# Optimization experiments

Hardware: AMD Instinct MI355X
Metric: run time of the kernel (lower is better)

The kernel has to match this reference:

```python
import jax, jax.numpy as jnp
import numpy as np

H, HKV, D = 32, 8, 128          # query heads, kv heads, head dim
G = H // HKV                     # GQA group size
PAGE, TOPK = 64, 64              # page size, top-k pages per (b, kv-head)
SCALE = D ** -0.5


def rotate_half(x):
    x1, x2 = x[..., : x.shape[-1] // 2], x[..., x.shape[-1] // 2 :]
    return jnp.concatenate((-x2, x1), axis=-1)


def setup_inputs() -> dict:
    key = jax.random.key(0)
    ks = jax.random.split(key, 8)
    B, Q, HID, S = 4, 1, 4096, 16384
    hidden_states = jax.random.normal(ks[0], (B, Q, HID), jnp.float32)
    # rotary embedding for current decode position S
    inv_freq = 1.0 / (10000.0 ** (np.arange(0, D, 2, dtype=np.float32) / D))
    ang = np.float32(S) * inv_freq
    emb = np.concatenate([ang, ang])  # [D]
    cos = jnp.broadcast_to(jnp.asarray(np.cos(emb))[None, None, :], (B, Q, D)).astype(jnp.float32)
    sin = jnp.broadcast_to(jnp.asarray(np.sin(emb))[None, None, :], (B, Q, D)).astype(jnp.float32)
    k_cache = jax.random.normal(ks[1], (B, HKV, S, D), jnp.float32)
    v_cache = jax.random.normal(ks[2], (B, HKV, S, D), jnp.float32)
    Wq = jax.random.normal(ks[3], (H * D, HID), jnp.float32) * 0.02
    Wk = jax.random.normal(ks[4], (HKV * D, HID), jnp.float32) * 0.02
    Wv = jax.random.normal(ks[5], (HKV * D, HID), jnp.float32) * 0.02
    Wo = jax.random.normal(ks[6], (HID, H * D), jnp.float32) * 0.02
    return dict(hidden_states=hidden_states, cos=cos, sin=sin,
                k_cache=k_cache, v_cache=v_cache, Wq=Wq, Wk=Wk, Wv=Wv, Wo=Wo)


def reference(hidden_states, cos, sin, k_cache, v_cache, Wq, Wk, Wv, Wo):
    B, Q, HID = hidden_states.shape
    S = k_cache.shape[2]
    P = S // PAGE

    # QKV projections (Linear, no bias) -> [B, heads, Q, D]
    q = (hidden_states @ Wq.T).reshape(B, Q, H, D).transpose(0, 2, 1, 3)
    k_new = (hidden_states @ Wk.T).reshape(B, Q, HKV, D).transpose(0, 2, 1, 3)
    v_new = (hidden_states @ Wv.T).reshape(B, Q, HKV, D).transpose(0, 2, 1, 3)

    # RoPE (unsqueeze_dim=1)
    c, s = cos[:, None, :, :], sin[:, None, :, :]
    q = q * c + rotate_half(q) * s
    k_new = k_new * c + rotate_half(k_new) * s

    # merge grouped query heads to kv heads (reduce='mean', merge_mode='kv')
    q_merged = q.reshape(B, HKV, G, Q, D).mean(axis=2)[:, :, 0, :]  # [B, HKV, D]

    # Quest page summaries: per-page elementwise min/max of keys
    Kp = k_cache.reshape(B, HKV, P, PAGE, D)
    Vp = v_cache.reshape(B, HKV, P, PAGE, D)
    kmin = Kp.min(axis=3)  # [B, HKV, P, D]
    kmax = Kp.max(axis=3)
    qm = q_merged[:, :, None, :]
    page_scores = jnp.maximum(qm * kmin, qm * kmax).sum(axis=-1)  # [B, HKV, P]

    # top-k page selection per (batch, kv head), gather selected pages
    _, idx = jax.lax.top_k(page_scores, TOPK)  # [B, HKV, TOPK]
    gidx = idx[:, :, :, None, None]
    K_sel = jnp.take_along_axis(Kp, gidx, axis=2).reshape(B, HKV, TOPK * PAGE, D)
    V_sel = jnp.take_along_axis(Vp, gidx, axis=2).reshape(B, HKV, TOPK * PAGE, D)

    # append current decode token's kv
    K = jnp.concatenate([K_sel, k_new], axis=2)  # [B, HKV, L, D]
    V = jnp.concatenate([V_sel, v_new], axis=2)

    # GQA attention over gathered sparse KV (no mask in quest decode path)
    qg = q.reshape(B, HKV, G, Q, D)
    logits = jnp.einsum('bhgqd,bhld->bhgql', qg, K) * SCALE
    w = jax.nn.softmax(logits.astype(jnp.float32), axis=-1).astype(q.dtype)
    o = jnp.einsum('bhgql,bhld->bhgqd', w, V)              # [B, HKV, G, Q, D]
    o = o.reshape(B, H, Q, D).transpose(0, 2, 1, 3).reshape(B, Q, H * D)
    return o @ Wo.T  # [B, Q, HID]
```

## Files before the change

### kernel.cpp

```cpp
#include <hip/hip_runtime.h>
#include <hip/hip_bf16.h>
#include <math.h>

constexpr int NB    = 4;
constexpr int NHID  = 4096;
constexpr int NHEAD = 32;
constexpr int NKV   = 8;
constexpr int NGQ   = 4;
constexpr int ND    = 128;
constexpr int NS    = 16384;
constexpr int NPG   = 64;
constexpr int NP    = 256;
constexpr int NTOP  = 64;
constexpr int NSPLIT = 32;
constexpr int PPS   = NTOP / NSPLIT;
constexpr float FSCALE = 0.08838834764831845f;

__global__ __launch_bounds__(256) void k_qkv(
    const float* __restrict__ hs, const float* __restrict__ Wq,
    const float* __restrict__ Wk, const float* __restrict__ Wv,
    float* __restrict__ qkv) {
  int row0 = blockIdx.x * 4;
  int t = threadIdx.x;
  const float4* x4 = (const float4*)hs;
  const float4* wr[4];
#pragma unroll
  for (int r = 0; r < 4; r++) {
    int row = row0 + r;
    const float* w;
    if (row < 4096)      w = Wq + (size_t)row * NHID;
    else if (row < 5120) w = Wk + (size_t)(row - 4096) * NHID;
    else                 w = Wv + (size_t)(row - 5120) * NHID;
    wr[r] = (const float4*)w;
  }
  float acc[4][4] = {};
  for (int j = t; j < NHID / 4; j += 256) {
    float4 x0 = x4[j], x1 = x4[1024 + j], x2 = x4[2048 + j], x3 = x4[3072 + j];
#pragma unroll
    for (int r = 0; r < 4; r++) {
      float4 w4 = wr[r][j];
      acc[r][0] += w4.x * x0.x + w4.y * x0.y + w4.z * x0.z + w4.w * x0.w;
      acc[r][1] += w4.x * x1.x + w4.y * x1.y + w4.z * x1.z + w4.w * x1.w;
      acc[r][2] += w4.x * x2.x + w4.y * x2.y + w4.z * x2.z + w4.w * x2.w;
      acc[r][3] += w4.x * x3.x + w4.y * x3.y + w4.z * x3.z + w4.w * x3.w;
    }
  }
  __shared__ float red[4][16];
  int lane = t & 63, wv = t >> 6;
#pragma unroll
  for (int r = 0; r < 4; r++)
#pragma unroll
    for (int b = 0; b < 4; b++) {
      float v = acc[r][b];
      v += __shfl_down(v, 32); v += __shfl_down(v, 16); v += __shfl_down(v, 8);
      v += __shfl_down(v, 4);  v += __shfl_down(v, 2);  v += __shfl_down(v, 1);
      if (lane == 0) red[wv][r * 4 + b] = v;
    }
  __syncthreads();
  if (t < 16) {
    int r = t >> 2, b = t & 3;
    float s = red[0][t] + red[1][t] + red[2][t] + red[3][t];
    qkv[(size_t)b * 6144 + row0 + r] = s;
  }
}

__global__ __launch_bounds__(256) void k_rope_merge(
    const float* __restrict__ qkv, const float* __restrict__ cosp,
    const float* __restrict__ sinp, float* __restrict__ qr,
    float* __restrict__ kn, float* __restrict__ vn, float* __restrict__ qm) {
  int b = blockIdx.x >> 3, kv = blockIdx.x & 7;
  const float* cs = cosp + b * ND;
  const float* sn = sinp + b * ND;
  int t = threadIdx.x;
  int g = t >> 6, i = t & 63;
  __shared__ float sq[4][ND];
  {
    int h = kv * NGQ + g;
    const float* q = qkv + (size_t)b * 6144 + h * ND;
    float x1 = q[i], x2 = q[i + 64];
    float o1 = x1 * cs[i] - x2 * sn[i];
    float o2 = x2 * cs[i + 64] + x1 * sn[i + 64];
    float* dst = qr + ((size_t)b * NHEAD + h) * ND;
    dst[i] = o1; dst[i + 64] = o2;
    sq[g][i] = o1; sq[g][i + 64] = o2;
  }
  if (t < 64) {
    const float* k = qkv + (size_t)b * 6144 + 4096 + kv * ND;
    float x1 = k[t], x2 = k[t + 64];
    float* dst = kn + ((size_t)b * NKV + kv) * ND;
    dst[t] = x1 * cs[t] - x2 * sn[t];
    dst[t + 64] = x2 * cs[t + 64] + x1 * sn[t + 64];
  }
  if (t < 128) {
    vn[((size_t)b * NKV + kv) * ND + t] = qkv[(size_t)b * 6144 + 5120 + kv * ND + t];
  }
  __syncthreads();
  if (t < 128) {
    qm[((size_t)b * NKV + kv) * ND + t] =
        0.25f * (sq[0][t] + sq[1][t] + sq[2][t] + sq[3][t]);
  }
}

__global__ __launch_bounds__(256) void k_pagescore(
    const float* __restrict__ kc, const float* __restrict__ qm,
    float* __restrict__ scores) {
  int bid = blockIdx.x;
  int p = bid & (NP - 1);
  int bh = bid >> 8;
  const float4* Kp = (const float4*)(kc + ((size_t)bh * NS + (size_t)p * NPG) * ND);
  int t = threadIdx.x;
  int c4 = t & 31, rg = t >> 5;
  float4 mn = make_float4(INFINITY, INFINITY, INFINITY, INFINITY);
  float4 mx = make_float4(-INFINITY, -INFINITY, -INFINITY, -INFINITY);
#pragma unroll
  for (int r = 0; r < 8; r++) {
    float4 v = Kp[(rg * 8 + r) * 32 + c4];
    mn.x = fminf(mn.x, v.x); mn.y = fminf(mn.y, v.y);
    mn.z = fminf(mn.z, v.z); mn.w = fminf(mn.w, v.w);
    mx.x = fmaxf(mx.x, v.x); mx.y = fmaxf(mx.y, v.y);
    mx.z = fmaxf(mx.z, v.z); mx.w = fmaxf(mx.w, v.w);
  }
  __shared__ float4 smn[8][32], smx[8][32];
  smn[rg][c4] = mn; smx[rg][c4] = mx;
  __syncthreads();
  if (t < 32) {
    float4 a = smn[0][t], b4 = smx[0][t];
#pragma unroll
    for (int r = 1; r < 8; r++) {
      float4 u = smn[r][t], w = smx[r][t];
      a.x = fminf(a.x, u.x); a.y = fminf(a.y, u.y);
      a.z = fminf(a.z, u.z); a.w = fminf(a.w, u.w);
      b4.x = fmaxf(b4.x, w.x); b4.y = fmaxf(b4.y, w.y);
      b4.z = fmaxf(b4.z, w.z); b4.w = fmaxf(b4.w, w.w);
    }
    const float4 qv = ((const float4*)(qm + (size_t)bh * ND))[t];
    float s = fmaxf(qv.x * a.x, qv.x * b4.x)
            + fmaxf(qv.y * a.y, qv.y * b4.y)
            + fmaxf(qv.z * a.z, qv.z * b4.z)
            + fmaxf(qv.w * a.w, qv.w * b4.w);
    s += __shfl_xor(s, 1); s += __shfl_xor(s, 2); s += __shfl_xor(s, 4);
    s += __shfl_xor(s, 8); s += __shfl_xor(s, 16);
    if (t == 0) scores[bid] = s;
  }
}

__global__ __launch_bounds__(256) void k_topk(
    const float* __restrict__ scores, int* __restrict__ sel) {
  int bh = blockIdx.x;
  int t = threadIdx.x;
  __shared__ float s[256];
  s[t] = scores[(size_t)bh * NP + t];
  __syncthreads();
  float mine = s[t];
  int rank = 0;
  for (int j = 0; j < 256; j++) {
    float v = s[j];
    rank += (v > mine) || (v == mine && j < t);
  }
  if (rank < NTOP) sel[(size_t)bh * NTOP + rank] = t;
}

__global__ __launch_bounds__(256) void k_attn_part(
    const float* __restrict__ kc, const float* __restrict__ vc,
    const float* __restrict__ qr, const int* __restrict__ sel,
    float* __restrict__ part_l, float* __restrict__ part_o) {
  int idx = blockIdx.x;
  int sp = idx & (NSPLIT - 1);
  int bh = idx / NSPLIT;
  int b = bh >> 3, kv = bh & 7;
  int t = threadIdx.x;
  int g = t >> 6, lane = t & 63;
  int h = kv * NGQ + g;
  int half = lane >> 5;
  int li = lane & 31;
  const float4* q4 = (const float4*)(qr + ((size_t)b * NHEAD + h) * ND);
  float4 qv = q4[li];
  float lsum = 0.f;
  float4 o = make_float4(0.f, 0.f, 0.f, 0.f);
  int page0 = sel[(size_t)bh * NTOP + sp * 2];
  int page1 = sel[(size_t)bh * NTOP + sp * 2 + 1];
  const float4* K0 = (const float4*)(kc + ((size_t)bh * NS + (size_t)page0 * NPG) * ND);
  const float4* V0 = (const float4*)(vc + ((size_t)bh * NS + (size_t)page0 * NPG) * ND);
  const float4* K1 = (const float4*)(kc + ((size_t)bh * NS + (size_t)page1 * NPG) * ND);
  const float4* V1 = (const float4*)(vc + ((size_t)bh * NS + (size_t)page1 * NPG) * ND);
  for (int r2 = 0; r2 < NPG / 2; r2++) {
    int r = r2 * 2 + half;
    float4 ka = K0[r * 32 + li];
    float4 kb = K1[r * 32 + li];
    float d0 = ka.x * qv.x + ka.y * qv.y + ka.z * qv.z + ka.w * qv.w;
    float d1 = kb.x * qv.x + kb.y * qv.y + kb.z * qv.z + kb.w * qv.w;
    d0 += __shfl_xor(d0, 1);  d1 += __shfl_xor(d1, 1);
    d0 += __shfl_xor(d0, 2);  d1 += __shfl_xor(d1, 2);
    d0 += __shfl_xor(d0, 4);  d1 += __shfl_xor(d1, 4);
    d0 += __shfl_xor(d0, 8);  d1 += __shfl_xor(d1, 8);
    d0 += __shfl_xor(d0, 16); d1 += __shfl_xor(d1, 16);
    float w0 = __expf(d0 * FSCALE);
    float w1 = __expf(d1 * FSCALE);
    lsum += w0 + w1;
    float4 va = V0[r * 32 + li];
    float4 vb = V1[r * 32 + li];
    o.x += w0 * va.x + w1 * vb.x;
    o.y += w0 * va.y + w1 * vb.y;
    o.z += w0 * va.z + w1 * vb.z;
    o.w += w0 * va.w + w1 * vb.w;
  }
  o.x += __shfl_xor(o.x, 32); o.y += __shfl_xor(o.y, 32);
  o.z += __shfl_xor(o.z, 32); o.w += __shfl_xor(o.w, 32);
  lsum += __shfl_xor(lsum, 32);
  if (half == 0) {
    float4* po = (float4*)(part_o + (((size_t)bh * NGQ + g) * NSPLIT + sp) * ND);
    po[li] = o;
    if (li == 0) part_l[((size_t)bh * NGQ + g) * NSPLIT + sp] = lsum;
  }
}

__global__ __launch_bounds__(64) void k_combine(
    const float* __restrict__ qr, const float* __restrict__ kn,
    const float* __restrict__ vn, const float* __restrict__ part_l,
    const float* __restrict__ part_o, float* __restrict__ attno) {
  int bid = blockIdx.x;
  int b = bid >> 5, h = bid & 31;
  int kv = h >> 2, g = h & 3;
  int lane = threadIdx.x;
  int bh = b * NKV + kv;
  const float2* q2 = (const float2*)(qr + ((size_t)b * NHEAD + h) * ND);
  const float2* k2 = (const float2*)(kn + (size_t)bh * ND);
  float2 qv = q2[lane], kk = k2[lane];
  float d = qv.x * kk.x + qv.y * kk.y;
  d += __shfl_xor(d, 1); d += __shfl_xor(d, 2); d += __shfl_xor(d, 4);
  d += __shfl_xor(d, 8); d += __shfl_xor(d, 16); d += __shfl_xor(d, 32);
  float wn = __expf(d * FSCALE);
  const float2* v2 = (const float2*)(vn + (size_t)bh * ND);
  float2 vv = v2[lane];
  float ox = wn * vv.x, oy = wn * vv.y, lt = wn;
  const float* pl = part_l + ((size_t)bh * NGQ + g) * NSPLIT;
  const float2* po = (const float2*)(part_o + (((size_t)bh * NGQ + g) * NSPLIT) * ND);
  for (int s = 0; s < NSPLIT; s++) {
    lt += pl[s];
    float2 p = po[(size_t)s * 64 + lane];
    ox += p.x; oy += p.y;
  }
  float inv = 1.0f / lt;
  float2* ao = (float2*)(attno + ((size_t)b * NHEAD + h) * ND);
  ao[lane] = make_float2(ox * inv, oy * inv);
}

__global__ __launch_bounds__(256) void k_oproj(
    const float* __restrict__ Wo, const float* __restrict__ x,
    float* __restrict__ out) {
  int row0 = blockIdx.x * 4;
  int t = threadIdx.x;
  const float4* x4 = (const float4*)x;
  float acc[4][4] = {};
  for (int j = t; j < NHID / 4; j += 256) {
    float4 x0 = x4[j], x1 = x4[1024 + j], x2 = x4[2048 + j], x3 = x4[3072 + j];
#pragma unroll
    for (int r = 0; r < 4; r++) {
      float4 w4 = ((const float4*)(Wo + (size_t)(row0 + r) * NHID))[j];
      acc[r][0] += w4.x * x0.x + w4.y * x0.y + w4.z * x0.z + w4.w * x0.w;
      acc[r][1] += w4.x * x1.x + w4.y * x1.y + w4.z * x1.z + w4.w * x1.w;
      acc[r][2] += w4.x * x2.x + w4.y * x2.y + w4.z * x2.z + w4.w * x2.w;
      acc[r][3] += w4.x * x3.x + w4.y * x3.y + w4.z * x3.z + w4.w * x3.w;
    }
  }
  __shared__ float red[4][16];
  int lane = t & 63, wv = t >> 6;
#pragma unroll
  for (int r = 0; r < 4; r++)
#pragma unroll
    for (int b = 0; b < 4; b++) {
      float v = acc[r][b];
      v += __shfl_down(v, 32); v += __shfl_down(v, 16); v += __shfl_down(v, 8);
      v += __shfl_down(v, 4);  v += __shfl_down(v, 2);  v += __shfl_down(v, 1);
      if (lane == 0) red[wv][r * 4 + b] = v;
    }
  __syncthreads();
  if (t < 16) {
    int r = t >> 2, b = t & 3;
    float s = red[0][t] + red[1][t] + red[2][t] + red[3][t];
    out[(size_t)b * NHID + row0 + r] = s;
  }
}

extern "C" void kernel_launch(void* const* d_in, const int* in_sizes, int n_in,
                              void* d_out, int out_size, void* d_ws, size_t ws_size,
                              hipStream_t stream) {
  const float* hs   = (const float*)d_in[0];
  const float* cosp = (const float*)d_in[1];
  const float* sinp = (const float*)d_in[2];
  const float* kc   = (const float*)d_in[3];
  const float* vc   = (const float*)d_in[4];
  const float* Wq   = (const float*)d_in[5];
  const float* Wk   = (const float*)d_in[6];
  const float* Wv   = (const float*)d_in[7];
  const float* Wo   = (const float*)d_in[8];
  float* out = (float*)d_out;

  float* ws = (float*)d_ws;
  float* qkv    = ws;
  float* qr     = ws + 24576;
  float* kn     = ws + 40960;
  float* vn     = ws + 45056;
  float* qm     = ws + 49152;
  float* scores = ws + 53248;
  int*   sel    = (int*)(ws + 61440);
  float* part_l = ws + 63488;
  float* part_o = ws + 67584;
  float* attno  = ws + 591872;

  k_qkv<<<6144 / 4, 256, 0, stream>>>(hs, Wq, Wk, Wv, qkv);
  k_rope_merge<<<NB * NKV, 256, 0, stream>>>(qkv, cosp, sinp, qr, kn, vn, qm);
  k_pagescore<<<NB * NKV * NP, 256, 0, stream>>>(kc, qm, scores);
  k_topk<<<NB * NKV, 256, 0, stream>>>(scores, sel);
  k_attn_part<<<NB * NKV * NSPLIT, 256, 0, stream>>>(kc, vc, qr, sel, part_l, part_o);
  k_combine<<<NB * NHEAD, 64, 0, stream>>>(qr, kn, vn, part_l, part_o, attno);
  k_oproj<<<NHID / 4, 256, 0, stream>>>(Wo, attno, out);
}
```

Before: 128.4 us.

## Fuse RoPE/merge and top-k into consumer kernels, dropping two launches

Removes the standalone rope/merge and top-k kernels. RoPE and the group-mean are recomputed inside the page-score, attention and combine kernels, and each attention block ranks the page scores itself to find its two pages. The aim is to save two launches and their intermediate buffers. The cost is redundant work: every page-score block recomputes the merged query, and every attention block runs a 256-way rank.

Result: no change. 127.2 us (-1.0%).

```diff
diff --git a/kernel.cpp b/kernel.cpp
--- a/kernel.cpp
+++ b/kernel.cpp
@@ -13,7 +13,6 @@
 constexpr int NP    = 256;
 constexpr int NTOP  = 64;
 constexpr int NSPLIT = 32;
-constexpr int PPS   = NTOP / NSPLIT;
 constexpr float FSCALE = 0.08838834764831845f;
 
 __global__ __launch_bounds__(256) void k_qkv(
@@ -64,51 +63,32 @@
   }
 }
 
-__global__ __launch_bounds__(256) void k_rope_merge(
-    const float* __restrict__ qkv, const float* __restrict__ cosp,
-    const float* __restrict__ sinp, float* __restrict__ qr,
-    float* __restrict__ kn, float* __restrict__ vn, float* __restrict__ qm) {
-  int b = blockIdx.x >> 3, kv = blockIdx.x & 7;
-  const float* cs = cosp + b * ND;
-  const float* sn = sinp + b * ND;
-  int t = threadIdx.x;
-  int g = t >> 6, i = t & 63;
-  __shared__ float sq[4][ND];
-  {
-    int h = kv * NGQ + g;
-    const float* q = qkv + (size_t)b * 6144 + h * ND;
-    float x1 = q[i], x2 = q[i + 64];
-    float o1 = x1 * cs[i] - x2 * sn[i];
-    float o2 = x2 * cs[i + 64] + x1 * sn[i + 64];
-    float* dst = qr + ((size_t)b * NHEAD + h) * ND;
-    dst[i] = o1; dst[i + 64] = o2;
-    sq[g][i] = o1; sq[g][i + 64] = o2;
-  }
-  if (t < 64) {
-    const float* k = qkv + (size_t)b * 6144 + 4096 + kv * ND;
-    float x1 = k[t], x2 = k[t + 64];
-    float* dst = kn + ((size_t)b * NKV + kv) * ND;
-    dst[t] = x1 * cs[t] - x2 * sn[t];
-    dst[t + 64] = x2 * cs[t + 64] + x1 * sn[t + 64];
-  }
-  if (t < 128) {
-    vn[((size_t)b * NKV + kv) * ND + t] = qkv[(size_t)b * 6144 + 5120 + kv * ND + t];
-  }
-  __syncthreads();
-  if (t < 128) {
-    qm[((size_t)b * NKV + kv) * ND + t] =
-        0.25f * (sq[0][t] + sq[1][t] + sq[2][t] + sq[3][t]);
-  }
-}
-
 __global__ __launch_bounds__(256) void k_pagescore(
-    const float* __restrict__ kc, const float* __restrict__ qm,
+    const float* __restrict__ kc, const float* __restrict__ qkv,
+    const float* __restrict__ cosp, const float* __restrict__ sinp,
     float* __restrict__ scores) {
   int bid = blockIdx.x;
   int p = bid & (NP - 1);
   int bh = bid >> 8;
+  int b = bh >> 3, kv = bh & 7;
+  int t = threadIdx.x;
+  __shared__ float sq[4][ND];
+  __shared__ __align__(16) float qmS[ND];
+  {
+    int g = t >> 6, i = t & 63;
+    int h = kv * NGQ + g;
+    const float* cs = cosp + b * ND;
+    const float* sn = sinp + b * ND;
+    const float* q = qkv + (size_t)b * 6144 + h * ND;
+    float x1 = q[i], x2 = q[i + 64];
+    sq[g][i]      = x1 * cs[i] - x2 * sn[i];
+    sq[g][i + 64] = x2 * cs[i + 64] + x1 * sn[i + 64];
+  }
+  __syncthreads();
+  if (t < 128) {
+    qmS[t] = 0.25f * (sq[0][t] + sq[1][t] + sq[2][t] + sq[3][t]);
+  }
   const float4* Kp = (const float4*)(kc + ((size_t)bh * NS + (size_t)p * NPG) * ND);
-  int t = threadIdx.x;
   int c4 = t & 31, rg = t >> 5;
   float4 mn = make_float4(INFINITY, INFINITY, INFINITY, INFINITY);
   float4 mx = make_float4(-INFINITY, -INFINITY, -INFINITY, -INFINITY);
@@ -133,7 +113,7 @@
       b4.x = fmaxf(b4.x, w.x); b4.y = fmaxf(b4.y, w.y);
       b4.z = fmaxf(b4.z, w.z); b4.w = fmaxf(b4.w, w.w);
     }
-    const float4 qv = ((const float4*)(qm + (size_t)bh * ND))[t];
+    const float4 qv = ((const float4*)qmS)[t];
     float s = fmaxf(qv.x * a.x, qv.x * b4.x)
             + fmaxf(qv.y * a.y, qv.y * b4.y)
             + fmaxf(qv.z * a.z, qv.z * b4.z)
@@ -144,25 +124,10 @@
   }
 }
 
-__global__ __launch_bounds__(256) void k_topk(
-    const float* __restrict__ scores, int* __restrict__ sel) {
-  int bh = blockIdx.x;
-  int t = threadIdx.x;
-  __shared__ float s[256];
-  s[t] = scores[(size_t)bh * NP + t];
-  __syncthreads();
-  float mine = s[t];
-  int rank = 0;
-  for (int j = 0; j < 256; j++) {
-    float v = s[j];
-    rank += (v > mine) || (v == mine && j < t);
-  }
-  if (rank < NTOP) sel[(size_t)bh * NTOP + rank] = t;
-}
-
 __global__ __launch_bounds__(256) void k_attn_part(
     const float* __restrict__ kc, const float* __restrict__ vc,
-    const float* __restrict__ qr, const int* __restrict__ sel,
+    const float* __restrict__ qkv, const float* __restrict__ cosp,
+    const float* __restrict__ sinp, const float* __restrict__ scores,
     float* __restrict__ part_l, float* __restrict__ part_o) {
   int idx = blockIdx.x;
   int sp = idx & (NSPLIT - 1);
@@ -173,16 +138,41 @@
   int h = kv * NGQ + g;
   int half = lane >> 5;
   int li = lane & 31;
-  const float4* q4 = (const float4*)(qr + ((size_t)b * NHEAD + h) * ND);
-  float4 qv = q4[li];
-  float lsum = 0.f;
-  float4 o = make_float4(0.f, 0.f, 0.f, 0.f);
-  int page0 = sel[(size_t)bh * NTOP + sp * 2];
-  int page1 = sel[(size_t)bh * NTOP + sp * 2 + 1];
+  __shared__ float s_sc[NP];
+  __shared__ int s_pg[2];
+  if (t < NP) s_sc[t] = scores[(size_t)bh * NP + t];
+  __syncthreads();
+  {
+    float mine = s_sc[t];
+    int rank = 0;
+    for (int j = 0; j < NP; j++) {
+      float v = s_sc[j];
+      rank += (v > mine) || (v == mine && j < t);
+    }
+    if (rank == sp * 2)     s_pg[0] = t;
+    if (rank == sp * 2 + 1) s_pg[1] = t;
+  }
+  float4 qv;
+  {
+    const float4* q4 = (const float4*)(qkv + (size_t)b * 6144 + h * ND);
+    const float4* c4p = (const float4*)(cosp + b * ND);
+    const float4* s4p = (const float4*)(sinp + b * ND);
+    float4 qa = q4[li], qp = q4[li ^ 16];
+    float4 cc = c4p[li], ss = s4p[li];
+    float sgn = (li < 16) ? -1.f : 1.f;
+    qv.x = qa.x * cc.x + sgn * qp.x * ss.x;
+    qv.y = qa.y * cc.y + sgn * qp.y * ss.y;
+    qv.z = qa.z * cc.z + sgn * qp.z * ss.z;
+    qv.w = qa.w * cc.w + sgn * qp.w * ss.w;
+  }
+  __syncthreads();
+  int page0 = s_pg[0], page1 = s_pg[1];
   const float4* K0 = (const float4*)(kc + ((size_t)bh * NS + (size_t)page0 * NPG) * ND);
   const float4* V0 = (const float4*)(vc + ((size_t)bh * NS + (size_t)page0 * NPG) * ND);
   const float4* K1 = (const float4*)(kc + ((size_t)bh * NS + (size_t)page1 * NPG) * ND);
   const float4* V1 = (const float4*)(vc + ((size_t)bh * NS + (size_t)page1 * NPG) * ND);
+  float lsum = 0.f;
+  float4 o = make_float4(0.f, 0.f, 0.f, 0.f);
   for (int r2 = 0; r2 < NPG / 2; r2++) {
     int r = r2 * 2 + half;
     float4 ka = K0[r * 32 + li];
@@ -215,22 +205,33 @@
 }
 
 __global__ __launch_bounds__(64) void k_combine(
-    const float* __restrict__ qr, const float* __restrict__ kn,
-    const float* __restrict__ vn, const float* __restrict__ part_l,
+    const float* __restrict__ qkv, const float* __restrict__ cosp,
+    const float* __restrict__ sinp, const float* __restrict__ part_l,
     const float* __restrict__ part_o, float* __restrict__ attno) {
   int bid = blockIdx.x;
   int b = bid >> 5, h = bid & 31;
   int kv = h >> 2, g = h & 3;
   int lane = threadIdx.x;
   int bh = b * NKV + kv;
-  const float2* q2 = (const float2*)(qr + ((size_t)b * NHEAD + h) * ND);
-  const float2* k2 = (const float2*)(kn + (size_t)bh * ND);
-  float2 qv = q2[lane], kk = k2[lane];
+  const float2* c2p = (const float2*)(cosp + b * ND);
+  const float2* s2p = (const float2*)(sinp + b * ND);
+  float2 cc = c2p[lane], ss = s2p[lane];
+  float sgn = (lane < 32) ? -1.f : 1.f;
+  const float2* q2 = (const float2*)(qkv + (size_t)b * 6144 + h * ND);
+  float2 qa = q2[lane], qp = q2[lane ^ 32];
+  float2 qv;
+  qv.x = qa.x * cc.x + sgn * qp.x * ss.x;
+  qv.y = qa.y * cc.y + sgn * qp.y * ss.y;
+  const float2* k2 = (const float2*)(qkv + (size_t)b * 6144 + 4096 + kv * ND);
+  float2 ka = k2[lane], kp = k2[lane ^ 32];
+  float2 kk;
+  kk.x = ka.x * cc.x + sgn * kp.x * ss.x;
+  kk.y = ka.y * cc.y + sgn * kp.y * ss.y;
   float d = qv.x * kk.x + qv.y * kk.y;
   d += __shfl_xor(d, 1); d += __shfl_xor(d, 2); d += __shfl_xor(d, 4);
   d += __shfl_xor(d, 8); d += __shfl_xor(d, 16); d += __shfl_xor(d, 32);
   float wn = __expf(d * FSCALE);
-  const float2* v2 = (const float2*)(vn + (size_t)bh * ND);
+  const float2* v2 = (const float2*)(qkv + (size_t)b * 6144 + 5120 + kv * ND);
   float2 vv = v2[lane];
   float ox = wn * vv.x, oy = wn * vv.y, lt = wn;
   const float* pl = part_l + ((size_t)bh * NGQ + g) * NSPLIT;
@@ -298,21 +299,14 @@
 
   float* ws = (float*)d_ws;
   float* qkv    = ws;
-  float* qr     = ws + 24576;
-  float* kn     = ws + 40960;
-  float* vn     = ws + 45056;
-  float* qm     = ws + 49152;
-  float* scores = ws + 53248;
-  int*   sel    = (int*)(ws + 61440);
-  float* part_l = ws + 63488;
-  float* part_o = ws + 67584;
-  float* attno  = ws + 591872;
+  float* scores = ws + 24576;
+  float* part_l = ws + 32768;
+  float* part_o = ws + 36864;
+  float* attno  = ws + 561152;
 
   k_qkv<<<6144 / 4, 256, 0, stream>>>(hs, Wq, Wk, Wv, qkv);
-  k_rope_merge<<<NB * NKV, 256, 0, stream>>>(qkv, cosp, sinp, qr, kn, vn, qm);
-  k_pagescore<<<NB * NKV * NP, 256, 0, stream>>>(kc, qm, scores);
-  k_topk<<<NB * NKV, 256, 0, stream>>>(scores, sel);
-  k_attn_part<<<NB * NKV * NSPLIT, 256, 0, stream>>>(kc, vc, qr, sel, part_l, part_o);
-  k_combine<<<NB * NHEAD, 64, 0, stream>>>(qr, kn, vn, part_l, part_o, attno);
+  k_pagescore<<<NB * NKV * NP, 256, 0, stream>>>(kc, qkv, cosp, sinp, scores);
+  k_attn_part<<<NB * NKV * NSPLIT, 256, 0, stream>>>(kc, vc, qkv, cosp, sinp, scores, part_l, part_o);
+  k_combine<<<NB * NHEAD, 64, 0, stream>>>(qkv, cosp, sinp, part_l, part_o, attno);
   k_oproj<<<NHID / 4, 256, 0, stream>>>(Wo, attno, out);
 }
```
